# Kernel optimization log

Hardware: AMD Instinct MI355X
Metric: run time of the kernel (lower is better)

Reference implementation:

```python
import jax, jax.numpy as jnp
import numpy as np

B, C, D = 16384, 4096, 512
ALPHA = 0.1
BETA = 0.25


def setup_inputs() -> dict:
    key = jax.random.key(0)
    kx, kc = jax.random.split(key)
    x = jax.random.normal(kx, (B, D), dtype=jnp.float32)
    codes = jax.random.normal(kc, (1, C, D), dtype=jnp.float32)
    return {"x": x, "codes": codes}


def reference(x, codes):
    # x: (B, D), codes: (1, C, D). Eval-mode forward of Quantizer (l2 metric).
    d = x.shape[1]
    c = codes[0]                                  # (C, D)
    # squared l2 distance via expansion (same math as sum((x-c)^2, -1))
    x_sq = jnp.sum(x * x, axis=-1, keepdims=True)  # (B, 1)
    c_sq = jnp.sum(c * c, axis=-1)                 # (C,)
    dots = jnp.einsum('bd,cd->bc', x, c)           # (B, C)
    raw_distances = x_sq + c_sq[None, :] - 2.0 * dots
    distances = raw_distances / d / ALPHA          # scaling preserved for faithfulness
    indices = jnp.argmin(distances, axis=-1)       # (B,)
    quantized = c[indices]                         # (B, D) gather
    # commit loss: dist(x, stop_grad(quantized)); codebook loss: dist(stop_grad(x), quantized)
    diff_commit = x - jax.lax.stop_gradient(quantized)
    loss_commit = jnp.mean(jnp.sum(diff_commit * diff_commit, axis=-1))
    diff_code = jax.lax.stop_gradient(x) - quantized
    loss_codebook = jnp.mean(jnp.sum(diff_code * diff_code, axis=-1))
    loss = loss_commit + BETA * loss_codebook
    return quantized, indices, loss
```

## Files before the change

### kernel.cpp

```cpp
#include <hip/hip_runtime.h>

#define B_SZ 16384
#define C_SZ 4096
#define D_SZ 512

#define QSCALE 22.7f
#define INV_S2 (1.0f / (QSCALE * QSCALE))
#define EPS 6.0f
#define DBIAS 1024.0f

typedef __attribute__((ext_vector_type(4))) int intx4;

__device__ inline unsigned q4(const float4 v) {
    int a = (int)rintf(v.x * QSCALE); a = max(-127, min(127, a));
    int b = (int)rintf(v.y * QSCALE); b = max(-127, min(127, b));
    int c = (int)rintf(v.z * QSCALE); c = max(-127, min(127, c));
    int d = (int)rintf(v.w * QSCALE); d = max(-127, min(127, d));
    return ((unsigned)(a & 255)) | ((unsigned)(b & 255) << 8) |
           ((unsigned)(c & 255) << 16) | ((unsigned)(d & 255) << 24);
}
__device__ inline void gload16(const void* g, void* l) {
    __builtin_amdgcn_global_load_lds(
        (const __attribute__((address_space(1))) void*)g,
        (__attribute__((address_space(3))) void*)l, 16, 0, 0);
}

#define SCHEDB()  __builtin_amdgcn_sched_barrier(0)
#define VM0()     do { SCHEDB(); asm volatile("s_waitcnt vmcnt(0)"); SCHEDB(); } while (0)
#define LGKM0()   do { asm volatile("s_waitcnt lgkmcnt(0)"); SCHEDB(); } while (0)

#define ROR16(v, N) \
    ((unsigned)__builtin_amdgcn_update_dpp(0, (int)(v), 0x120 + (N), 0xF, 0xF, true))

__global__ __launch_bounds__(256) void convert_kernel(const float* __restrict__ x,
                                                      const float* __restrict__ codes,
                                                      unsigned* __restrict__ xq,
                                                      unsigned* __restrict__ cq,
                                                      float* __restrict__ csq,
                                                      float* __restrict__ xsq) {
    __shared__ float red[4];
    const int XB = (B_SZ * D_SZ) / 4 / 256;
    const int t = threadIdx.x;
    const int wave = t >> 6;
    const int lane = t & 63;
    if (blockIdx.x < XB) {
        const int tid = blockIdx.x * 256 + t;
        const float4 v = ((const float4*)x)[tid];
        xq[tid] = q4(v);
        float s = fmaf(v.x, v.x, fmaf(v.y, v.y, fmaf(v.z, v.z, v.w * v.w)));
        #pragma unroll
        for (int off = 32; off; off >>= 1) s += __shfl_down(s, off, 64);
        if (lane == 0) red[wave] = s;
        __syncthreads();
        if (t == 0) {
            xsq[blockIdx.x * 2]     = red[0] + red[1];
            xsq[blockIdx.x * 2 + 1] = red[2] + red[3];
        }
    } else {
        const int code = (blockIdx.x - XB) * 4 + wave;
        const float4* cp = (const float4*)(codes + (size_t)code * D_SZ);
        float s = 0.0f;
        #pragma unroll
        for (int u = 0; u < 2; ++u) {
            const float4 v = cp[lane + 64 * u];
            cq[(size_t)code * (D_SZ / 4) + lane + 64 * u] = q4(v);
            s = fmaf(v.x, v.x, s); s = fmaf(v.y, v.y, s);
            s = fmaf(v.z, v.z, s); s = fmaf(v.w, v.w, s);
        }
        #pragma unroll
        for (int off = 32; off; off >>= 1) s += __shfl_down(s, off, 64);
        if (lane == 0) csq[code] = s;
    }
}

__global__ __launch_bounds__(512, 1) void gemm_argmin_kernel(
        const unsigned char* __restrict__ xq,
        const unsigned char* __restrict__ cq,
        const float* __restrict__ csq,
        uint2* __restrict__ table) {
    __shared__ unsigned char sB[4][256][128];
    __shared__ unsigned char sA[128][128];

    const int t = threadIdx.x;
    const int wave = t >> 6;
    const int lane = t & 63;
    const int quad = lane >> 4;
    const int l15 = lane & 15;
    const int wm = wave >> 2;
    const int wn = wave & 3;

    const int rowbase0 = blockIdx.y * 512;
    const int colbase = blockIdx.x * 256;

    const int lrow = lane >> 3;
    const int lchunk = (lane & 7) ^ lrow;
    const unsigned char* gA0 = xq + (size_t)(rowbase0 + wave * 16 + lrow) * D_SZ + lchunk * 16;
    const unsigned char* gB0 = cq + (size_t)(colbase + wave * 32 + lrow) * D_SZ + lchunk * 16;

    float cs2[4];
    #pragma unroll
    for (int j = 0; j < 4; ++j)
        cs2[j] = fmaf(0.5f, csq[colbase + wn * 64 + j * 16 + l15], DBIAS);

#define STAGE_A(rt, kt) do { \
        const unsigned char* _g = gA0 + (size_t)(rt) * 128 * D_SZ + (kt) * 128; \
        gload16(_g,                    &sA[wave * 16][0]); \
        gload16(_g + (size_t)8 * D_SZ, &sA[wave * 16 + 8][0]); \
    } while (0)
#define STAGE_B(kt) do { \
        const unsigned char* _g = gB0 + (kt) * 128; \
        _Pragma("unroll") for (int u = 0; u < 4; ++u) \
            gload16(_g + (size_t)(u * 8) * D_SZ, &sB[kt][wave * 32 + u * 8][0]); \
    } while (0)
#define LDA_REGS() do { \
        _Pragma("unroll") for (int ks = 0; ks < 2; ++ks) { \
            const int cc = (((ks * 4 + quad) ^ (l15 & 7))) * 16; \
            _Pragma("unroll") for (int i = 0; i < 4; ++i) \
                areg[ks][i] = *(const intx4*)&sA[wm * 64 + i * 16 + l15][cc]; \
        } \
    } while (0)
#define COMPUTE_KT(kt) do { \
        _Pragma("unroll") for (int ks = 0; ks < 2; ++ks) { \
            const int cc = (((ks * 4 + quad) ^ (l15 & 7))) * 16; \
            intx4 b[4]; \
            _Pragma("unroll") for (int j = 0; j < 4; ++j) \
                b[j] = *(const intx4*)&sB[kt][wn * 64 + j * 16 + l15][cc]; \
            _Pragma("unroll") for (int i = 0; i < 4; ++i) \
                _Pragma("unroll") for (int j = 0; j < 4; ++j) \
                    acc[i][j] = __builtin_amdgcn_mfma_i32_16x16x64_i8(areg[ks][i], b[j], acc[i][j], 0, 0, 0); \
        } \
    } while (0)
#define MERGE_STEP(N) do { \
        const unsigned ok1 = ROR16(k1, N); \
        const unsigned ok2 = ROR16(k2, N); \
        const unsigned hi = max(k1, ok1); \
        const unsigned w2 = (k1 < ok1) ? k2 : ok2; \
        k1 = min(k1, ok1); \
        k2 = min(hi, w2); \
    } while (0)

    STAGE_B(0);
    STAGE_A(0, 0);
    VM0();
    __syncthreads();

    const int hb = blockIdx.x * 4 + wn;

    for (int rt = 0; rt < 4; ++rt) {
        intx4 acc[4][4];
        #pragma unroll
        for (int i = 0; i < 4; ++i)
            #pragma unroll
            for (int j = 0; j < 4; ++j) acc[i][j] = (intx4)0;

        #pragma unroll
        for (int kt = 0; kt < 4; ++kt) {
            intx4 areg[2][4];
            LDA_REGS();
            LGKM0();
            __syncthreads();
            if (kt < 3) STAGE_A(rt, kt + 1);
            else if (rt < 3) STAGE_A(rt + 1, 0);
            if (rt == 0 && kt < 3) STAGE_B(kt + 1);
            COMPUTE_KT(kt);
            VM0();
            __syncthreads();
        }

        #pragma unroll
        for (int i = 0; i < 4; ++i) {
            #pragma unroll
            for (int r = 0; r < 4; ++r) {
                unsigned k[4];
                #pragma unroll
                for (int j = 0; j < 4; ++j) {
                    const float d = fmaf(-(float)acc[i][j][r], INV_S2, cs2[j]);
                    k[j] = (__float_as_uint(d) & 0xFFFFFFC0u) | (unsigned)(j * 16 + l15);
                }
                const unsigned lo1 = min(k[0], k[1]), hi1 = max(k[0], k[1]);
                const unsigned lo2 = min(k[2], k[3]), hi2 = max(k[2], k[3]);
                unsigned k1 = min(lo1, lo2);
                unsigned k2 = min(max(lo1, lo2), min(hi1, hi2));
                MERGE_STEP(8); MERGE_STEP(4); MERGE_STEP(2); MERGE_STEP(1);
                if (l15 == 0) {
                    const int grow = rowbase0 + rt * 128 + wm * 64 + i * 16 + quad * 4 + r;
                    table[(size_t)grow * 64 + hb] = make_uint2(k1, k2);
                }
            }
        }
    }
#undef STAGE_A
#undef STAGE_B
#undef LDA_REGS
#undef COMPUTE_KT
#undef MERGE_STEP
}

__global__ __launch_bounds__(256) void rerank_gather_loss_kernel(
        const float* __restrict__ x,
        const float* __restrict__ codes,
        const float* __restrict__ csq,
        const float* __restrict__ xsq,
        const uint2* __restrict__ table,
        float* __restrict__ outq,
        float* __restrict__ out_idx_f,
        float* __restrict__ loss_slot) {
    __shared__ float red[4];
    const int t = threadIdx.x;
    const int wave = t >> 6;
    const int lane = t & 63;
    const int row0 = (blockIdx.x * 4 + wave) * 4;

    uint2 e[4];
    #pragma unroll
    for (int r = 0; r < 4; ++r)
        e[r] = table[(size_t)(row0 + r) * 64 + lane];

    int fin[4];
    float wsum = 0.0f;
    #pragma unroll
    for (int r = 0; r < 4; ++r) {
        const unsigned k1 = e[r].x, k2 = e[r].y;
        unsigned mk = k1;
        #pragma unroll
        for (int off = 32; off; off >>= 1)
            mk = min(mk, (unsigned)__shfl_xor((int)mk, off, 64));

        const float thr = __uint_as_float(mk & 0xFFFFFFC0u) + EPS;
        const float v1 = __uint_as_float(k1 & 0xFFFFFFC0u);
        const float v2 = __uint_as_float(k2 & 0xFFFFFFC0u);
        const unsigned long long b1 = __ballot(v1 <= thr);
        const unsigned long long b2 = __ballot(v2 <= thr);

        const unsigned long long bm = __ballot(k1 == mk);
        fin[r] = (__ffsll(bm) - 1) * 64 + (int)(mk & 63u);
        float distp = __uint_as_float(mk & 0xFFFFFFC0u) - DBIAS;

        if (__popcll(b1) + __popcll(b2) > 1) {
            const float4* xp = (const float4*)(x + (size_t)(row0 + r) * D_SZ);
            const float4 xv0 = xp[lane];
            const float4 xv1 = xp[lane + 64];
            const int c1 = lane * 64 + (int)(k1 & 63u);
            const int c2 = lane * 64 + (int)(k2 & 63u);
            float bv = 3.4e38f; int bi = 0x7FFFFFFF;
            #pragma unroll
            for (int pass = 0; pass < 2; ++pass) {
                unsigned long long bb = pass ? b2 : b1;
                const int myc = pass ? c2 : c1;
                while (bb) {
                    const int src = __ffsll((unsigned long long)bb) - 1;
                    bb &= bb - 1;
                    const int ci = __shfl(myc, src, 64);
                    const float4* cp = (const float4*)(codes + (size_t)ci * D_SZ);
                    const float4 c0 = cp[lane];
                    const float4 c1v = cp[lane + 64];
                    float s = 0.0f;
                    s = fmaf(xv0.x, c0.x, s);  s = fmaf(xv0.y, c0.y, s);
                    s = fmaf(xv0.z, c0.z, s);  s = fmaf(xv0.w, c0.w, s);
                    s = fmaf(xv1.x, c1v.x, s); s = fmaf(xv1.y, c1v.y, s);
                    s = fmaf(xv1.z, c1v.z, s); s = fmaf(xv1.w, c1v.w, s);
                    #pragma unroll
                    for (int off = 32; off; off >>= 1) s += __shfl_xor(s, off, 64);
                    const float d = fmaf(0.5f, csq[ci], -s);
                    if (d < bv || (d == bv && ci < bi)) { bv = d; bi = ci; }
                }
            }
            fin[r] = bi;
            distp = bv;
        }
        wsum += xsq[row0 + r] + 2.0f * distp;
    }

    float4 qv[4][2];
    #pragma unroll
    for (int r = 0; r < 4; ++r) {
        const float4* qp = (const float4*)(codes + (size_t)fin[r] * D_SZ);
        qv[r][0] = qp[lane];
        qv[r][1] = qp[lane + 64];
    }

    #pragma unroll
    for (int r = 0; r < 4; ++r) {
        float4* op = (float4*)(outq + (size_t)(row0 + r) * D_SZ);
        op[lane] = qv[r][0];
        op[lane + 64] = qv[r][1];
        if (lane == 0) out_idx_f[row0 + r] = (float)fin[r];
    }

    if (lane == 0) red[wave] = wsum;
    __syncthreads();
    if (t == 0)
        atomicAdd(loss_slot, (red[0] + red[1] + red[2] + red[3]) * (1.25f / (float)B_SZ));
}

extern "C" void kernel_launch(void* const* d_in, const int* in_sizes, int n_in,
                              void* d_out, int out_size, void* d_ws, size_t ws_size,
                              hipStream_t stream) {
    const float* x = (const float*)d_in[0];
    const float* codes = (const float*)d_in[1];

    float* outq = (float*)d_out;
    float* out_idx_f = outq + (size_t)B_SZ * D_SZ;
    float* loss_slot = out_idx_f + B_SZ;

    unsigned char* xq = (unsigned char*)d_ws;
    unsigned char* cq = xq + (size_t)B_SZ * D_SZ;
    float* csq = (float*)(cq + (size_t)C_SZ * D_SZ);
    uint2* table = (uint2*)(csq + C_SZ);
    float* xsq = (float*)(table + (size_t)B_SZ * 64);

    const int XB = (B_SZ * D_SZ) / 4 / 256;
    const int CB = C_SZ / 4;
    convert_kernel<<<XB + CB, 256, 0, stream>>>(x, codes, (unsigned*)xq, (unsigned*)cq, csq, xsq);
    gemm_argmin_kernel<<<dim3(C_SZ / 256, B_SZ / 512), 512, 0, stream>>>(xq, cq, csq, table);
    rerank_gather_loss_kernel<<<B_SZ / 16, 256, 0, stream>>>(x, codes, csq, xsq, table, outq, out_idx_f, loss_slot);
}
```

Measured before the change: 167.4 us.

## Compute loss directly from x minus quantized; replace atomic with two-stage reduction

The per-row x squared-norm reduction and its shuffle/syncthreads are dropped from the convert kernel. The rerank kernel now preloads x rows for every row and computes the loss directly as the squared difference between x and the gathered code. The final atomicAdd is replaced by per-block partials and a single-block reduction kernel, which also makes the loss deterministic and no longer relies on the output slot being pre-zeroed. In exchange, every rerank block always reads its x rows and does extra ALU work, and the pipeline gains an extra kernel launch.

```diff
diff --git a/kernel.cpp b/kernel.cpp
--- a/kernel.cpp
+++ b/kernel.cpp
@@ -36,27 +36,16 @@
                                                       const float* __restrict__ codes,
                                                       unsigned* __restrict__ xq,
                                                       unsigned* __restrict__ cq,
-                                                      float* __restrict__ csq,
-                                                      float* __restrict__ xsq) {
-    __shared__ float red[4];
+                                                      float* __restrict__ csq) {
     const int XB = (B_SZ * D_SZ) / 4 / 256;
-    const int t = threadIdx.x;
-    const int wave = t >> 6;
-    const int lane = t & 63;
     if (blockIdx.x < XB) {
-        const int tid = blockIdx.x * 256 + t;
+        const int tid = blockIdx.x * 256 + threadIdx.x;
         const float4 v = ((const float4*)x)[tid];
         xq[tid] = q4(v);
-        float s = fmaf(v.x, v.x, fmaf(v.y, v.y, fmaf(v.z, v.z, v.w * v.w)));
-        #pragma unroll
-        for (int off = 32; off; off >>= 1) s += __shfl_down(s, off, 64);
-        if (lane == 0) red[wave] = s;
-        __syncthreads();
-        if (t == 0) {
-            xsq[blockIdx.x * 2]     = red[0] + red[1];
-            xsq[blockIdx.x * 2 + 1] = red[2] + red[3];
-        }
     } else {
+        const int t = threadIdx.x;
+        const int wave = t >> 6;
+        const int lane = t & 63;
         const int code = (blockIdx.x - XB) * 4 + wave;
         const float4* cp = (const float4*)(codes + (size_t)code * D_SZ);
         float s = 0.0f;
@@ -200,11 +189,10 @@
         const float* __restrict__ x,
         const float* __restrict__ codes,
         const float* __restrict__ csq,
-        const float* __restrict__ xsq,
         const uint2* __restrict__ table,
         float* __restrict__ outq,
         float* __restrict__ out_idx_f,
-        float* __restrict__ loss_slot) {
+        float* __restrict__ partials) {
     __shared__ float red[4];
     const int t = threadIdx.x;
     const int wave = t >> 6;
@@ -212,12 +200,16 @@
     const int row0 = (blockIdx.x * 4 + wave) * 4;
 
     uint2 e[4];
-    #pragma unroll
-    for (int r = 0; r < 4; ++r)
+    float4 xv[4][2];
+    #pragma unroll
+    for (int r = 0; r < 4; ++r) {
         e[r] = table[(size_t)(row0 + r) * 64 + lane];
+        const float4* xp = (const float4*)(x + (size_t)(row0 + r) * D_SZ);
+        xv[r][0] = xp[lane];
+        xv[r][1] = xp[lane + 64];
+    }
 
     int fin[4];
-    float wsum = 0.0f;
     #pragma unroll
     for (int r = 0; r < 4; ++r) {
         const unsigned k1 = e[r].x, k2 = e[r].y;
@@ -234,12 +226,8 @@
 
         const unsigned long long bm = __ballot(k1 == mk);
         fin[r] = (__ffsll(bm) - 1) * 64 + (int)(mk & 63u);
-        float distp = __uint_as_float(mk & 0xFFFFFFC0u) - DBIAS;
 
         if (__popcll(b1) + __popcll(b2) > 1) {
-            const float4* xp = (const float4*)(x + (size_t)(row0 + r) * D_SZ);
-            const float4 xv0 = xp[lane];
-            const float4 xv1 = xp[lane + 64];
             const int c1 = lane * 64 + (int)(k1 & 63u);
             const int c2 = lane * 64 + (int)(k2 & 63u);
             float bv = 3.4e38f; int bi = 0x7FFFFFFF;
@@ -255,10 +243,10 @@
                     const float4 c0 = cp[lane];
                     const float4 c1v = cp[lane + 64];
                     float s = 0.0f;
-                    s = fmaf(xv0.x, c0.x, s);  s = fmaf(xv0.y, c0.y, s);
-                    s = fmaf(xv0.z, c0.z, s);  s = fmaf(xv0.w, c0.w, s);
-                    s = fmaf(xv1.x, c1v.x, s); s = fmaf(xv1.y, c1v.y, s);
-                    s = fmaf(xv1.z, c1v.z, s); s = fmaf(xv1.w, c1v.w, s);
+                    s = fmaf(xv[r][0].x, c0.x, s);  s = fmaf(xv[r][0].y, c0.y, s);
+                    s = fmaf(xv[r][0].z, c0.z, s);  s = fmaf(xv[r][0].w, c0.w, s);
+                    s = fmaf(xv[r][1].x, c1v.x, s); s = fmaf(xv[r][1].y, c1v.y, s);
+                    s = fmaf(xv[r][1].z, c1v.z, s); s = fmaf(xv[r][1].w, c1v.w, s);
                     #pragma unroll
                     for (int off = 32; off; off >>= 1) s += __shfl_xor(s, off, 64);
                     const float d = fmaf(0.5f, csq[ci], -s);
@@ -266,9 +254,7 @@
                 }
             }
             fin[r] = bi;
-            distp = bv;
         }
-        wsum += xsq[row0 + r] + 2.0f * distp;
     }
 
     float4 qv[4][2];
@@ -279,18 +265,41 @@
         qv[r][1] = qp[lane + 64];
     }
 
+    float s = 0.0f;
     #pragma unroll
     for (int r = 0; r < 4; ++r) {
         float4* op = (float4*)(outq + (size_t)(row0 + r) * D_SZ);
         op[lane] = qv[r][0];
         op[lane + 64] = qv[r][1];
+        const float d0 = xv[r][0].x - qv[r][0].x, d1 = xv[r][0].y - qv[r][0].y;
+        const float d2 = xv[r][0].z - qv[r][0].z, d3 = xv[r][0].w - qv[r][0].w;
+        const float d4 = xv[r][1].x - qv[r][1].x, d5 = xv[r][1].y - qv[r][1].y;
+        const float d6 = xv[r][1].z - qv[r][1].z, d7 = xv[r][1].w - qv[r][1].w;
+        s += d0 * d0 + d1 * d1 + d2 * d2 + d3 * d3 + d4 * d4 + d5 * d5 + d6 * d6 + d7 * d7;
         if (lane == 0) out_idx_f[row0 + r] = (float)fin[r];
     }
-
-    if (lane == 0) red[wave] = wsum;
+    #pragma unroll
+    for (int off = 32; off; off >>= 1) s += __shfl_down(s, off, 64);
+    if (lane == 0) red[wave] = s;
+    __syncthreads();
+    if (t == 0) partials[blockIdx.x] = red[0] + red[1] + red[2] + red[3];
+}
+
+__global__ __launch_bounds__(256) void loss_reduce_kernel(const float* __restrict__ partials,
+                                                          float* __restrict__ loss_slot) {
+    __shared__ float red[4];
+    const int t = threadIdx.x;
+    const int wave = t >> 6;
+    const int lane = t & 63;
+    float s = 0.0f;
+    #pragma unroll
+    for (int i = 0; i < (B_SZ / 16) / 256; ++i) s += partials[i * 256 + t];
+    #pragma unroll
+    for (int off = 32; off; off >>= 1) s += __shfl_down(s, off, 64);
+    if (lane == 0) red[wave] = s;
     __syncthreads();
     if (t == 0)
-        atomicAdd(loss_slot, (red[0] + red[1] + red[2] + red[3]) * (1.25f / (float)B_SZ));
+        *loss_slot = (red[0] + red[1] + red[2] + red[3]) * (1.25f / (float)B_SZ);
 }
 
 extern "C" void kernel_launch(void* const* d_in, const int* in_sizes, int n_in,
@@ -307,11 +316,12 @@
     unsigned char* cq = xq + (size_t)B_SZ * D_SZ;
     float* csq = (float*)(cq + (size_t)C_SZ * D_SZ);
     uint2* table = (uint2*)(csq + C_SZ);
-    float* xsq = (float*)(table + (size_t)B_SZ * 64);
+    float* partials = (float*)(table + (size_t)B_SZ * 64);
 
     const int XB = (B_SZ * D_SZ) / 4 / 256;
     const int CB = C_SZ / 4;
-    convert_kernel<<<XB + CB, 256, 0, stream>>>(x, codes, (unsigned*)xq, (unsigned*)cq, csq, xsq);
+    convert_kernel<<<XB + CB, 256, 0, stream>>>(x, codes, (unsigned*)xq, (unsigned*)cq, csq);
     gemm_argmin_kernel<<<dim3(C_SZ / 256, B_SZ / 512), 512, 0, stream>>>(xq, cq, csq, table);
-    rerank_gather_loss_kernel<<<B_SZ / 16, 256, 0, stream>>>(x, codes, csq, xsq, table, outq, out_idx_f, loss_slot);
-}
+    rerank_gather_loss_kernel<<<B_SZ / 16, 256, 0, stream>>>(x, codes, csq, table, outq, out_idx_f, partials);
+    loss_reduce_kernel<<<1, 256, 0, stream>>>(partials, loss_slot);
+}
```

After: 164.6 us (median of 2 runs). Within noise of the previous version (-1.6%).
